# Kernel tuning notes

Measured on AMD Instinct MI355X. Metric: run time of the kernel, lower is better.

The kernel has to match this reference:

```python
import jax, jax.numpy as jnp
import numpy as np

WINDOW_SIZE = 11
N_CHANNELS = 3
SIGMA = 1.5
K1, K2 = 0.01, 0.03
VALUE_RANGE = 1.0


def _create_window(window_size: int, n_channels: int, sigma: float) -> np.ndarray:
    # 1D gaussian, normalized, then outer product -> 2D kernel
    coords = np.arange(window_size, dtype=np.float32) - (window_size - 1) / 2.0
    g = np.exp(-(coords ** 2) / (2.0 * sigma ** 2))
    g = g / g.sum()
    k2d = np.outer(g, g).astype(np.float32)  # (K, K), sums to 1
    # depthwise kernel, OIHW with I=1 (groups = n_channels)
    return np.broadcast_to(k2d, (n_channels, 1, window_size, window_size)).copy()


def _dwconv(x, window):
    # depthwise valid conv, NCHW / OIHW
    return jax.lax.conv_general_dilated(
        x, window, window_strides=(1, 1), padding='VALID',
        feature_group_count=window.shape[0],
        dimension_numbers=('NCHW', 'OIHW', 'NCHW'))


def setup_inputs() -> dict:
    key = jax.random.key(0)
    kx, ky = jax.random.split(key)
    N, C, H, W = 32, N_CHANNELS, 512, 512
    x = jax.random.uniform(kx, (N, C, H, W), dtype=jnp.float32)
    y = jax.random.uniform(ky, (N, C, H, W), dtype=jnp.float32)
    window = jnp.asarray(_create_window(WINDOW_SIZE, N_CHANNELS, SIGMA))
    return {"x": x, "y": y, "window": window}


def reference(x, y, window):
    c1 = (K1 * VALUE_RANGE) ** 2
    c2 = (K2 * VALUE_RANGE) ** 2

    mu_x = _dwconv(x, window)
    mu_y = _dwconv(y, window)
    mu_x_sq = mu_x ** 2
    mu_y_sq = mu_y ** 2
    mu_xy = mu_x * mu_y

    sigma_x_sq = _dwconv(x * x, window) - mu_x_sq
    sigma_y_sq = _dwconv(y * y, window) - mu_y_sq
    sigma_xy = _dwconv(x * y, window) - mu_xy

    cs = (2.0 * sigma_xy + c2) / (sigma_x_sq + sigma_y_sq + c2)
    ss = (2.0 * mu_xy + c1) / (mu_x_sq + mu_y_sq + c1) * cs

    l = ss.mean(axis=(-1, -2))  # (N, C) per-channel SSIM
    l = l.mean(axis=-1)         # (N,)  per-sample
    return l.mean()             # reduction='mean'
```

## Files before the change

### kernel.cpp

```cpp
#include <hip/hip_runtime.h>

#define KS    11
#define HH    512
#define WW    512
#define OUTD  502
#define OH    33
#define ROWS  44
#define NB    16
#define NIMG  96
#define PADW  524

__global__ __launch_bounds__(256, 2)
void ssim_main(const float* __restrict__ xg, const float* __restrict__ yg,
               const float* __restrict__ win, double* __restrict__ acc_out)
{
    __shared__ float shs[2][PADW];
    __shared__ float shd[2][PADW];
    __shared__ float wsums[4];

    const int tid  = threadIdx.x;
    const int img  = blockIdx.x % NIMG;
    const int band = blockIdx.x / NIMG;
    const int row0 = band * OH;
    const int c0   = 2 * tid;

    float g[6];
    #pragma unroll
    for (int i = 0; i < 6; i++) {
        float s = 0.f;
        #pragma unroll
        for (int j = 0; j < KS; j++) s += win[i * KS + j];
        g[i] = s;
    }
#define G(j) g[(j) <= 5 ? (j) : 10 - (j)]

    if (tid < (PADW - WW)) {
        shs[0][WW + tid] = 0.f; shs[1][WW + tid] = 0.f;
        shd[0][WW + tid] = 0.f; shd[1][WW + tid] = 0.f;
    }

    const float* xi = xg + (size_t)img * HH * WW;
    const float* yi = yg + (size_t)img * HH * WW;

    float acc[4][2][KS];
    #pragma unroll
    for (int q = 0; q < 4; q++)
        #pragma unroll
        for (int c = 0; c < 2; c++)
            #pragma unroll
            for (int s = 0; s < KS; s++) acc[q][c][s] = 0.f;

    float ssum = 0.f;

    const float C1x2 = 0.0002f;
    const float C2x2 = 0.0018f;

    float2 pfs, pfd;
    {
        int gr = row0; if (gr > HH - 1) gr = HH - 1;
        float2 ax = *(const float2*)&xi[(size_t)gr * WW + c0];
        float2 ay = *(const float2*)&yi[(size_t)gr * WW + c0];
        shs[0][c0] = ax.x + ay.x; shs[0][c0 + 1] = ax.y + ay.y;
        shd[0][c0] = ax.x - ay.x; shd[0][c0 + 1] = ax.y - ay.y;
        gr = row0 + 1; if (gr > HH - 1) gr = HH - 1;
        ax = *(const float2*)&xi[(size_t)gr * WW + c0];
        ay = *(const float2*)&yi[(size_t)gr * WW + c0];
        pfs = make_float2(ax.x + ay.x, ax.y + ay.y);
        pfd = make_float2(ax.x - ay.x, ax.y - ay.y);
    }
    __syncthreads();

    #pragma unroll 1
    for (int rb = 0; rb < ROWS / KS; rb++) {
        #pragma unroll
        for (int rr = 0; rr < KS; rr++) {
            const int r = rb * KS + rr;

            const float* sb = shs[r & 1];
            const float* db = shd[r & 1];
            float sv[12], dv[12];
            #pragma unroll
            for (int k = 0; k < 6; k++) {
                float2 a = *(const float2*)&sb[c0 + 2 * k];
                float2 b = *(const float2*)&db[c0 + 2 * k];
                sv[2 * k] = a.x; sv[2 * k + 1] = a.y;
                dv[2 * k] = b.x; dv[2 * k + 1] = b.y;
            }

            if (r + 1 < ROWS) {
                float* sw = shs[(r + 1) & 1];
                float* dw = shd[(r + 1) & 1];
                sw[c0] = pfs.x; sw[c0 + 1] = pfs.y;
                dw[c0] = pfd.x; dw[c0 + 1] = pfd.y;
            }
            if (r + 2 < ROWS) {
                int gr = row0 + r + 2; if (gr > HH - 1) gr = HH - 1;
                float2 ax = *(const float2*)&xi[(size_t)gr * WW + c0];
                float2 ay = *(const float2*)&yi[(size_t)gr * WW + c0];
                pfs = make_float2(ax.x + ay.x, ax.y + ay.y);
                pfd = make_float2(ax.x - ay.x, ax.y - ay.y);
            }

            float h0a = 0.f, h0b = 0.f, h1a = 0.f, h1b = 0.f;
            float h2a = 0.f, h2b = 0.f, h3a = 0.f, h3b = 0.f;
            float ts = sv[0] * sv[0];
            float td = dv[0] * dv[0];
            #pragma unroll
            for (int j = 0; j < KS; j++) {
                const float gj  = G(j);
                const float tsn = sv[j + 1] * sv[j + 1];
                const float tdn = dv[j + 1] * dv[j + 1];
                h0a = fmaf(gj, sv[j],     h0a); h0b = fmaf(gj, sv[j + 1], h0b);
                h1a = fmaf(gj, dv[j],     h1a); h1b = fmaf(gj, dv[j + 1], h1b);
                h2a = fmaf(gj, ts,        h2a); h2b = fmaf(gj, tsn,       h2b);
                h3a = fmaf(gj, td,        h3a); h3b = fmaf(gj, td = tdn,  h3b);
                ts = tsn;
            }

            {
                const float g0 = G(0);
                acc[0][0][rr] = g0 * h0a; acc[0][1][rr] = g0 * h0b;
                acc[1][0][rr] = g0 * h1a; acc[1][1][rr] = g0 * h1b;
                acc[2][0][rr] = g0 * h2a; acc[2][1][rr] = g0 * h2b;
                acc[3][0][rr] = g0 * h3a; acc[3][1][rr] = g0 * h3b;
            }
            #pragma unroll
            for (int i = 1; i < KS; i++) {
                const int slot = (rr - i + KS) % KS;
                const float gi = G(i);
                acc[0][0][slot] = fmaf(gi, h0a, acc[0][0][slot]);
                acc[0][1][slot] = fmaf(gi, h0b, acc[0][1][slot]);
                acc[1][0][slot] = fmaf(gi, h1a, acc[1][0][slot]);
                acc[1][1][slot] = fmaf(gi, h1b, acc[1][1][slot]);
                acc[2][0][slot] = fmaf(gi, h2a, acc[2][0][slot]);
                acc[2][1][slot] = fmaf(gi, h2b, acc[2][1][slot]);
                acc[3][0][slot] = fmaf(gi, h3a, acc[3][0][slot]);
                acc[3][1][slot] = fmaf(gi, h3b, acc[3][1][slot]);
            }

            const int es   = (rr + 1) % KS;
            const int jloc = r - (KS - 1);
            if (jloc >= 0 && jloc < OH && (row0 + jloc) < OUTD) {
                #pragma unroll
                for (int c = 0; c < 2; c++) {
                    if (c0 + c < OUTD) {
                        const float ms = acc[0][c][es], md = acc[1][c][es];
                        const float Ss = acc[2][c][es], Sd = acc[3][c][es];
                        const float a = ms * ms, b = md * md;
                        const float P = a - b;
                        const float Q = a + b;
                        const float U = Ss - Sd;
                        const float V = Ss + Sd;
                        const float num = (P + C1x2) * ((U - P) + C2x2);
                        const float den = (Q + C1x2) * ((V - Q) + C2x2);
                        float rc = __builtin_amdgcn_rcpf(den);
                        rc = rc * fmaf(-den, rc, 2.0f);
                        ssum = fmaf(num, rc, ssum);
                    }
                }
            }

            __syncthreads();
        }
    }

    #pragma unroll
    for (int off = 32; off > 0; off >>= 1)
        ssum += __shfl_down(ssum, off);
    const int wave = tid >> 6;
    if ((tid & 63) == 0) wsums[wave] = ssum;
    __syncthreads();
    if (tid == 0) {
        float s = wsums[0] + wsums[1] + wsums[2] + wsums[3];
        atomicAdd(acc_out, (double)s);
    }
}

__global__ void ssim_finalize(const double* __restrict__ acc, float* __restrict__ out)
{
    out[0] = (float)(acc[0] * (1.0 / 24192384.0));
}

extern "C" void kernel_launch(void* const* d_in, const int* in_sizes, int n_in,
                              void* d_out, int out_size, void* d_ws, size_t ws_size,
                              hipStream_t stream)
{
    const float* x   = (const float*)d_in[0];
    const float* y   = (const float*)d_in[1];
    const float* win = (const float*)d_in[2];
    float* out = (float*)d_out;
    double* acc = (double*)d_ws;

    hipMemsetAsync(acc, 0, sizeof(double), stream);
    ssim_main<<<dim3(NIMG * NB), dim3(256), 0, stream>>>(x, y, win, acc);
    ssim_finalize<<<dim3(1), dim3(1), 0, stream>>>(acc, out);
}
```

Baseline: 282.8 us.

## Use single-wave column-strip blocks without barriers and spread atomic accumulators

Each block becomes one 64-thread wavefront covering a 128-column strip plus an 11-column halo and a taller 45-row band. This removes every per-row __syncthreads and cuts the vertical halo overhead, at the cost of extra horizontal halo loads. The final reduction now spreads its atomic adds over up to 256 double slots that a 64-thread finalize kernel sums, reducing contention on one address. Correctness relies on lockstep execution within a wavefront to order the double-buffered LDS writes and reads, since no barrier or fence is left.

```diff
diff --git a/kernel.cpp b/kernel.cpp
--- a/kernel.cpp
+++ b/kernel.cpp
@@ -1,28 +1,35 @@
 #include <hip/hip_runtime.h>
 
-#define KS    11
-#define HH    512
-#define WW    512
-#define OUTD  502
-#define OH    33
-#define ROWS  44
-#define NB    16
-#define NIMG  96
-#define PADW  524
-
-__global__ __launch_bounds__(256, 2)
+#define KS     11
+#define HH     512
+#define WW     512
+#define OUTD   502
+#define OH     45
+#define ROWS   55
+#define NBANDS 12
+#define NSTRIP 4
+#define SCOLS  128
+#define LCOLS  140
+#define NIMG   96
+#define NACC   256
+
+__global__ __launch_bounds__(64, 2)
 void ssim_main(const float* __restrict__ xg, const float* __restrict__ yg,
-               const float* __restrict__ win, double* __restrict__ acc_out)
+               const float* __restrict__ win, double* __restrict__ acc_out,
+               const int accmask)
 {
-    __shared__ float shs[2][PADW];
-    __shared__ float shd[2][PADW];
-    __shared__ float wsums[4];
-
-    const int tid  = threadIdx.x;
-    const int img  = blockIdx.x % NIMG;
-    const int band = blockIdx.x / NIMG;
-    const int row0 = band * OH;
-    const int c0   = 2 * tid;
+    __shared__ float shs[2][LCOLS];
+    __shared__ float shd[2][LCOLS];
+
+    const int tid   = threadIdx.x;
+    const int bid   = blockIdx.x;
+    const int strip = bid & (NSTRIP - 1);
+    const int band  = (bid >> 2) % NBANDS;
+    const int img   = bid / (NSTRIP * NBANDS);
+    const int row0  = band * OH;
+    const int colb  = strip * SCOLS;
+    const int c0    = colb + 2 * tid;
+    const int l0    = 2 * tid;
 
     float g[6];
     #pragma unroll
@@ -34,13 +41,12 @@
     }
 #define G(j) g[(j) <= 5 ? (j) : 10 - (j)]
 
-    if (tid < (PADW - WW)) {
-        shs[0][WW + tid] = 0.f; shs[1][WW + tid] = 0.f;
-        shd[0][WW + tid] = 0.f; shd[1][WW + tid] = 0.f;
-    }
-
-    const float* xi = xg + (size_t)img * HH * WW;
-    const float* yi = yg + (size_t)img * HH * WW;
+    const float* xi = xg + (size_t)img * (HH * WW);
+    const float* yi = yg + (size_t)img * (HH * WW);
+
+    const bool hn = (tid < (LCOLS - SCOLS) / 2);
+    int hcol = colb + SCOLS + 2 * tid;
+    if (hcol > WW - 2) hcol = WW - 2;
 
     float acc[4][2][KS];
     #pragma unroll
@@ -51,24 +57,35 @@
             for (int s = 0; s < KS; s++) acc[q][c][s] = 0.f;
 
     float ssum = 0.f;
-
     const float C1x2 = 0.0002f;
     const float C2x2 = 0.0018f;
 
-    float2 pfs, pfd;
+    float2 pfs, pfd, phs, phd;
     {
-        int gr = row0; if (gr > HH - 1) gr = HH - 1;
-        float2 ax = *(const float2*)&xi[(size_t)gr * WW + c0];
-        float2 ay = *(const float2*)&yi[(size_t)gr * WW + c0];
-        shs[0][c0] = ax.x + ay.x; shs[0][c0 + 1] = ax.y + ay.y;
-        shd[0][c0] = ax.x - ay.x; shd[0][c0 + 1] = ax.y - ay.y;
-        gr = row0 + 1; if (gr > HH - 1) gr = HH - 1;
-        ax = *(const float2*)&xi[(size_t)gr * WW + c0];
-        ay = *(const float2*)&yi[(size_t)gr * WW + c0];
+        int gr = row0;
+        float2 ax = *(const float2*)&xi[gr * WW + c0];
+        float2 ay = *(const float2*)&yi[gr * WW + c0];
+        shs[0][l0] = ax.x + ay.x; shs[0][l0 + 1] = ax.y + ay.y;
+        shd[0][l0] = ax.x - ay.x; shd[0][l0 + 1] = ax.y - ay.y;
+        if (hn) {
+            float2 bx = *(const float2*)&xi[gr * WW + hcol];
+            float2 by = *(const float2*)&yi[gr * WW + hcol];
+            shs[0][SCOLS + l0] = bx.x + by.x; shs[0][SCOLS + l0 + 1] = bx.y + by.y;
+            shd[0][SCOLS + l0] = bx.x - by.x; shd[0][SCOLS + l0 + 1] = bx.y - by.y;
+        }
+        gr = row0 + 1;
+        ax = *(const float2*)&xi[gr * WW + c0];
+        ay = *(const float2*)&yi[gr * WW + c0];
         pfs = make_float2(ax.x + ay.x, ax.y + ay.y);
         pfd = make_float2(ax.x - ay.x, ax.y - ay.y);
+        phs = make_float2(0.f, 0.f); phd = make_float2(0.f, 0.f);
+        if (hn) {
+            float2 bx = *(const float2*)&xi[gr * WW + hcol];
+            float2 by = *(const float2*)&yi[gr * WW + hcol];
+            phs = make_float2(bx.x + by.x, bx.y + by.y);
+            phd = make_float2(bx.x - by.x, bx.y - by.y);
+        }
     }
-    __syncthreads();
 
     #pragma unroll 1
     for (int rb = 0; rb < ROWS / KS; rb++) {
@@ -81,8 +98,8 @@
             float sv[12], dv[12];
             #pragma unroll
             for (int k = 0; k < 6; k++) {
-                float2 a = *(const float2*)&sb[c0 + 2 * k];
-                float2 b = *(const float2*)&db[c0 + 2 * k];
+                float2 a = *(const float2*)&sb[l0 + 2 * k];
+                float2 b = *(const float2*)&db[l0 + 2 * k];
                 sv[2 * k] = a.x; sv[2 * k + 1] = a.y;
                 dv[2 * k] = b.x; dv[2 * k + 1] = b.y;
             }
@@ -90,15 +107,25 @@
             if (r + 1 < ROWS) {
                 float* sw = shs[(r + 1) & 1];
                 float* dw = shd[(r + 1) & 1];
-                sw[c0] = pfs.x; sw[c0 + 1] = pfs.y;
-                dw[c0] = pfd.x; dw[c0 + 1] = pfd.y;
+                sw[l0] = pfs.x; sw[l0 + 1] = pfs.y;
+                dw[l0] = pfd.x; dw[l0 + 1] = pfd.y;
+                if (hn) {
+                    sw[SCOLS + l0] = phs.x; sw[SCOLS + l0 + 1] = phs.y;
+                    dw[SCOLS + l0] = phd.x; dw[SCOLS + l0 + 1] = phd.y;
+                }
             }
             if (r + 2 < ROWS) {
                 int gr = row0 + r + 2; if (gr > HH - 1) gr = HH - 1;
-                float2 ax = *(const float2*)&xi[(size_t)gr * WW + c0];
-                float2 ay = *(const float2*)&yi[(size_t)gr * WW + c0];
+                float2 ax = *(const float2*)&xi[gr * WW + c0];
+                float2 ay = *(const float2*)&yi[gr * WW + c0];
                 pfs = make_float2(ax.x + ay.x, ax.y + ay.y);
                 pfd = make_float2(ax.x - ay.x, ax.y - ay.y);
+                if (hn) {
+                    float2 bx = *(const float2*)&xi[gr * WW + hcol];
+                    float2 by = *(const float2*)&yi[gr * WW + hcol];
+                    phs = make_float2(bx.x + by.x, bx.y + by.y);
+                    phd = make_float2(bx.x - by.x, bx.y - by.y);
+                }
             }
 
             float h0a = 0.f, h0b = 0.f, h1a = 0.f, h1b = 0.f;
@@ -113,8 +140,8 @@
                 h0a = fmaf(gj, sv[j],     h0a); h0b = fmaf(gj, sv[j + 1], h0b);
                 h1a = fmaf(gj, dv[j],     h1a); h1b = fmaf(gj, dv[j + 1], h1b);
                 h2a = fmaf(gj, ts,        h2a); h2b = fmaf(gj, tsn,       h2b);
-                h3a = fmaf(gj, td,        h3a); h3b = fmaf(gj, td = tdn,  h3b);
-                ts = tsn;
+                h3a = fmaf(gj, td,        h3a); h3b = fmaf(gj, tdn,       h3b);
+                ts = tsn; td = tdn;
             }
 
             {
@@ -159,26 +186,26 @@
                     }
                 }
             }
-
-            __syncthreads();
         }
     }
 
     #pragma unroll
     for (int off = 32; off > 0; off >>= 1)
         ssum += __shfl_down(ssum, off);
-    const int wave = tid >> 6;
-    if ((tid & 63) == 0) wsums[wave] = ssum;
-    __syncthreads();
-    if (tid == 0) {
-        float s = wsums[0] + wsums[1] + wsums[2] + wsums[3];
-        atomicAdd(acc_out, (double)s);
-    }
+    if (tid == 0)
+        atomicAdd(&acc_out[bid & accmask], (double)ssum);
 }
 
-__global__ void ssim_finalize(const double* __restrict__ acc, float* __restrict__ out)
+__global__ void ssim_finalize(const double* __restrict__ acc, float* __restrict__ out,
+                              const int nacc)
 {
-    out[0] = (float)(acc[0] * (1.0 / 24192384.0));
+    double s = 0.0;
+    for (int i = threadIdx.x; i < nacc; i += 64) s += acc[i];
+    #pragma unroll
+    for (int off = 32; off > 0; off >>= 1)
+        s += __shfl_down(s, off);
+    if (threadIdx.x == 0)
+        out[0] = (float)(s * (1.0 / 24192384.0));
 }
 
 extern "C" void kernel_launch(void* const* d_in, const int* in_sizes, int n_in,
@@ -191,7 +218,9 @@
     float* out = (float*)d_out;
     double* acc = (double*)d_ws;
 
-    hipMemsetAsync(acc, 0, sizeof(double), stream);
-    ssim_main<<<dim3(NIMG * NB), dim3(256), 0, stream>>>(x, y, win, acc);
-    ssim_finalize<<<dim3(1), dim3(1), 0, stream>>>(acc, out);
+    const int nacc = (ws_size >= NACC * sizeof(double)) ? NACC : 1;
+    hipMemsetAsync(acc, 0, nacc * sizeof(double), stream);
+    ssim_main<<<dim3(NIMG * NBANDS * NSTRIP), dim3(64), 0, stream>>>(
+        x, y, win, acc, nacc - 1);
+    ssim_finalize<<<dim3(1), dim3(64), 0, stream>>>(acc, out, nacc);
 }
```

New measurement: 329.4 us. 16.5% more time.
